# Kernel tuning notes

Measured on AMD Instinct MI355X. Metric: run time of the kernel, lower is better.

## Reference

```python
import jax, jax.numpy as jnp
import numpy as np

D = 1024
H = 16
DK = D // H


def apply_rope(x):
    # x: [B, H, T, dk]; interleaved-pair RoPE as in the torch source
    T, dim = x.shape[-2], x.shape[-1]
    inv_freq = 1.0 / (10000.0 ** (jnp.arange(0, dim, 2, dtype=x.dtype) / dim))  # [dk/2]
    pos = jnp.arange(T, dtype=x.dtype)
    sinusoid = pos[:, None] * inv_freq[None, :]  # [T, dk/2]
    sin, cos = jnp.sin(sinusoid), jnp.cos(sinusoid)
    x1, x2 = x[..., ::2], x[..., 1::2]
    rot = jnp.stack([x1 * cos - x2 * sin, x1 * sin + x2 * cos], axis=-1)
    return rot.reshape(x.shape)


def setup_inputs() -> dict:
    key = jax.random.key(0)
    k1, k2, k3, k4, k5 = jax.random.split(key, 5)
    B, T = 2, 2048
    s = 1.0 / np.sqrt(D)
    return {
        "x": jax.random.normal(k1, (B, T, D), dtype=jnp.float32),
        "W_qkv": jax.random.normal(k2, (D, 3 * D), dtype=jnp.float32) * s,
        "b_qkv": jnp.zeros((3 * D,), dtype=jnp.float32),
        "W_out": jax.random.normal(k3, (D, D), dtype=jnp.float32) * s,
        "b_out": jnp.zeros((D,), dtype=jnp.float32),
    }


def reference(x, W_qkv, b_qkv, W_out, b_out):
    B, T, C = x.shape
    qkv = x @ W_qkv + b_qkv  # [B, T, 3D]
    qkv = qkv.reshape(B, T, 3, H, DK).transpose(2, 0, 3, 1, 4)  # [3, B, H, T, dk]
    q, k, v = qkv[0], qkv[1], qkv[2]
    q, k = apply_rope(q), apply_rope(k)
    scores = jnp.einsum("bhtd,bhsd->bhts", q, k) / jnp.sqrt(jnp.asarray(DK, x.dtype))
    causal = jnp.tril(jnp.ones((T, T), dtype=bool))
    scores = jnp.where(causal, scores, jnp.asarray(-1e9, x.dtype))
    probs = jax.nn.softmax(scores, axis=-1)
    attn = jnp.einsum("bhts,bhsd->bhtd", probs, v)  # [B, H, T, dk]
    out = attn.transpose(0, 2, 1, 3).reshape(B, T, C)  # b h t d -> b t (h d)
    return out @ W_out + b_out
```

## Files before the change

### kernel.cpp

```cpp
#include <hip/hip_runtime.h>
#include <math.h>

#define DMODEL 1024
#define NHEAD  16
#define HDK    64
#define BATCH  2
#define SEQ    2048
#define MROWS  (BATCH*SEQ)
#define NQKV   (3*DMODEL)
#define LOG2_10000 13.287712379549449f
#define INV2PI 0.15915494309189535f
#define SCALE_LOG2E 0.1803368801111137f
#define M_FIX 8.0f

typedef __attribute__((ext_vector_type(8))) short bf16x8;
typedef __attribute__((ext_vector_type(4))) float f32x4;

__device__ __forceinline__ short f2bf(float f) {
    union { float f; unsigned u; } v; v.f = f;
    unsigned r = v.u + 0x7fffu + ((v.u >> 16) & 1u);
    return (short)(r >> 16);
}

__device__ __forceinline__ float fast_exp2(float x) {
#if __has_builtin(__builtin_amdgcn_exp2f)
    return __builtin_amdgcn_exp2f(x);
#else
    return exp2f(x);
#endif
}

__device__ __forceinline__ void gld_lds16(const short* g, short* l) {
    __builtin_amdgcn_global_load_lds(
        (const __attribute__((address_space(1))) void*)g,
        (__attribute__((address_space(3))) void*)l, 16, 0, 0);
}

__global__ __launch_bounds__(256) void prep_kernel(
    const float* __restrict__ x, const float* __restrict__ wqkv,
    const float* __restrict__ wout,
    short* __restrict__ xb, short* __restrict__ wqkv_t, short* __restrict__ wout_t)
{
    __shared__ short tile[32][33];
    const int tid = threadIdx.x;
    if (blockIdx.x < 2048) {
        const int i = (blockIdx.x * 256 + tid) * 8;
        float4 a = *(const float4*)(x + i);
        float4 b = *(const float4*)(x + i + 4);
        bf16x8 o;
        o[0] = f2bf(a.x); o[1] = f2bf(a.y); o[2] = f2bf(a.z); o[3] = f2bf(a.w);
        o[4] = f2bf(b.x); o[5] = f2bf(b.y); o[6] = f2bf(b.z); o[7] = f2bf(b.w);
        *(bf16x8*)(xb + i) = o;
        return;
    }
    const int bx = blockIdx.x - 2048;
    int nx = bx & 127;
    const int ky = bx >> 7;
    const float* in; short* out; int N;
    if (nx < 96) { in = wqkv; out = wqkv_t; N = NQKV; }
    else         { in = wout; out = wout_t; N = DMODEL; nx -= 96; }
    const int tx = tid & 31, ty = tid >> 5;
    const int n0 = nx * 32, k0 = ky * 32;
    #pragma unroll
    for (int i = 0; i < 32; i += 8)
        tile[ty + i][tx] = f2bf(in[(size_t)(k0 + ty + i) * N + n0 + tx]);
    __syncthreads();
    #pragma unroll
    for (int i = 0; i < 32; i += 8)
        out[(size_t)(n0 + ty + i) * DMODEL + k0 + tx] = tile[tx][ty + i];
}

__global__ __launch_bounds__(256) void qkv_gemm_kernel(
    const short* __restrict__ xb, const short* __restrict__ Wt,
    const float* __restrict__ bias,
    short* __restrict__ qd, short* __restrict__ kd, short* __restrict__ vtb)
{
    __shared__ __align__(16) short As[2][128 * 32];
    __shared__ __align__(16) short Bs[2][128 * 32];
    const int tid = threadIdx.x;
    const int lane = tid & 63, wave = tid >> 6;
    const int wm = wave & 1, wn = wave >> 1;
    const int l15 = lane & 15, quad = lane >> 4;
    const int n0 = blockIdx.x * 128, m0 = blockIdx.y * 128;
    const int srow = lane >> 2, sc = lane & 3;

    const short* gA1 = xb + (size_t)(m0 + wave * 32 + srow) * DMODEL + sc * 8;
    const short* gA2 = gA1 + (size_t)16 * DMODEL;
    const short* gB1 = Wt + (size_t)(n0 + wave * 32 + srow) * DMODEL + sc * 8;
    const short* gB2 = gB1 + (size_t)16 * DMODEL;
    const int lofsA1 = (wave * 32) * 32;
    const int lofsA2 = (wave * 32 + 16) * 32;

    f32x4 zero = {0.f, 0.f, 0.f, 0.f};
    f32x4 acc[4][4];
    #pragma unroll
    for (int i = 0; i < 4; ++i)
        #pragma unroll
        for (int j = 0; j < 4; ++j) acc[i][j] = zero;

    gld_lds16(gA1, As[0] + lofsA1);
    gld_lds16(gA2, As[0] + lofsA2);
    gld_lds16(gB1, Bs[0] + lofsA1);
    gld_lds16(gB2, Bs[0] + lofsA2);
    __syncthreads();

    for (int k = 0; k < DMODEL / 32; ++k) {
        const int cur = k & 1;
        if (k + 1 < DMODEL / 32) {
            const int kn = (k + 1) * 32;
            gld_lds16(gA1 + kn, As[cur ^ 1] + lofsA1);
            gld_lds16(gA2 + kn, As[cur ^ 1] + lofsA2);
            gld_lds16(gB1 + kn, Bs[cur ^ 1] + lofsA1);
            gld_lds16(gB2 + kn, Bs[cur ^ 1] + lofsA2);
        }
        bf16x8 af[4], bfr[4];
        #pragma unroll
        for (int i = 0; i < 4; ++i)
            af[i] = *(const bf16x8*)&As[cur][(wm * 64 + i * 16 + l15) * 32 + quad * 8];
        #pragma unroll
        for (int j = 0; j < 4; ++j)
            bfr[j] = *(const bf16x8*)&Bs[cur][(wn * 64 + j * 16 + l15) * 32 + quad * 8];
        #pragma unroll
        for (int i = 0; i < 4; ++i)
            #pragma unroll
            for (int j = 0; j < 4; ++j)
                acc[i][j] = __builtin_amdgcn_mfma_f32_16x16x32_bf16(af[i], bfr[j], acc[i][j], 0, 0, 0);
        __syncthreads();
    }

    const int which = n0 >> 10;
    float biasv[4], invf[4];
    int hh[4], dd[4];
    #pragma unroll
    for (int j = 0; j < 4; ++j) {
        const int n = n0 + wn * 64 + j * 16 + l15;
        biasv[j] = bias[n];
        hh[j] = (n & 1023) >> 6;
        dd[j] = n & 63;
        invf[j] = INV2PI * exp2f(-((float)(dd[j] & ~1) / 64.f) * LOG2_10000);
    }
    #pragma unroll
    for (int i = 0; i < 4; ++i) {
        #pragma unroll
        for (int r = 0; r < 4; ++r) {
            const int m = m0 + wm * 64 + i * 16 + quad * 4 + r;
            const int b = m >> 11, t = m & (SEQ - 1);
            #pragma unroll
            for (int j = 0; j < 4; ++j) {
                float val = acc[i][j][r] + biasv[j];
                if (which < 2) {
                    const float rev = (float)t * invf[j];
                    const float fr = rev - floorf(rev);
                    const float s = __builtin_amdgcn_sinf(fr);
                    const float c = __builtin_amdgcn_cosf(fr);
                    const float partner = __shfl_xor(val, 1);
                    val = (lane & 1) ? (partner * s + val * c) : (val * c - partner * s);
                    short* dst = (which == 0) ? qd : kd;
                    dst[((size_t)(b * NHEAD + hh[j]) * SEQ + t) * HDK + dd[j]] = f2bf(val);
                } else {
                    vtb[((size_t)(b * NHEAD + hh[j]) * HDK + dd[j]) * SEQ + t] = f2bf(val);
                }
            }
        }
    }
}

__global__ __launch_bounds__(256) void attn_mfma_kernel(
    const short* __restrict__ qd, const short* __restrict__ kd,
    const short* __restrict__ vt, short* __restrict__ od)
{
    __shared__ __align__(16) short Ks[2][2][64 * 32];
    __shared__ __align__(16) short Vs[2][2][64 * 32];
    __shared__ __align__(16) short Ps[4][16][64];
    const int tid = threadIdx.x, lane = tid & 63, w = tid >> 6;
    const int l15 = lane & 15, quad = lane >> 4;
    const int id = (int)blockIdx.x;
    const int c = id & 7, kblk = id >> 3;
    const int qt = 31 - (kblk & 31);
    const int jj = kblk >> 5;
    const int hb = c + 8 * jj;
    const int h = hb & 15, b = hb >> 4;
    const size_t base = ((size_t)(b * NHEAD + h)) * SEQ * HDK;
    const int srow = tid >> 2, sc = tid & 3;
    const int lofs = tid * 8;
    f32x4 zero = {0.f, 0.f, 0.f, 0.f};

    const short* kp0 = kd + base + (size_t)srow * HDK + sc * 8;
    const short* vp0 = vt + base + (size_t)srow * SEQ + sc * 8;
    const short* kp1 = kp0 + (size_t)64 * HDK;
    const short* vp1 = vp0 + 64;

    const int q0 = qt * 64;
    bf16x8 qf[2];
    {
        const short* qrow = qd + base + (size_t)(q0 + w * 16 + l15) * HDK;
        qf[0] = *(const bf16x8*)(qrow + quad * 8);
        qf[1] = *(const bf16x8*)(qrow + 32 + quad * 8);
    }
    float l_acc[4] = {0.f, 0.f, 0.f, 0.f};
    f32x4 o[4];
    #pragma unroll
    for (int j = 0; j < 4; ++j) o[j] = zero;

    const int nkt = qt + 1;
    const int npair = (nkt + 1) >> 1;

    bf16x8 rk[2][2], rv[2][2];
    rk[0][0] = *(const bf16x8*)kp0; rk[0][1] = *(const bf16x8*)(kp0 + 32);
    rv[0][0] = *(const bf16x8*)vp0; rv[0][1] = *(const bf16x8*)(vp0 + 32);
    rk[1][0] = *(const bf16x8*)kp1; rk[1][1] = *(const bf16x8*)(kp1 + 32);
    rv[1][0] = *(const bf16x8*)vp1; rv[1][1] = *(const bf16x8*)(vp1 + 32);

    for (int p = 0; p < npair; ++p) {
        __syncthreads();
        *(bf16x8*)&Ks[0][0][lofs] = rk[0][0]; *(bf16x8*)&Ks[0][1][lofs] = rk[0][1];
        *(bf16x8*)&Vs[0][0][lofs] = rv[0][0]; *(bf16x8*)&Vs[0][1][lofs] = rv[0][1];
        *(bf16x8*)&Ks[1][0][lofs] = rk[1][0]; *(bf16x8*)&Ks[1][1][lofs] = rk[1][1];
        *(bf16x8*)&Vs[1][0][lofs] = rv[1][0]; *(bf16x8*)&Vs[1][1][lofs] = rv[1][1];
        __syncthreads();
        if (p + 1 < npair) {
            const int sn = (2 * p + 2) * 64;
            const short* kn = kd + base + (size_t)(sn + srow) * HDK + sc * 8;
            const short* vn = vt + base + (size_t)srow * SEQ + sn + sc * 8;
            rk[0][0] = *(const bf16x8*)kn; rk[0][1] = *(const bf16x8*)(kn + 32);
            rv[0][0] = *(const bf16x8*)vn; rv[0][1] = *(const bf16x8*)(vn + 32);
            const short* kn2 = kn + (size_t)64 * HDK;
            const short* vn2 = vn + 64;
            rk[1][0] = *(const bf16x8*)kn2; rk[1][1] = *(const bf16x8*)(kn2 + 32);
            rv[1][0] = *(const bf16x8*)vn2; rv[1][1] = *(const bf16x8*)(vn2 + 32);
        }

        #pragma unroll
        for (int tt = 0; tt < 2; ++tt) {
            const int kt = 2 * p + tt;
            if (tt == 1 && kt >= nkt) break;
            f32x4 sacc[4];
            #pragma unroll
            for (int j = 0; j < 4; ++j) {
                bf16x8 kf0 = *(const bf16x8*)&Ks[tt][0][(j * 16 + l15) * 32 + quad * 8];
                bf16x8 kf1 = *(const bf16x8*)&Ks[tt][1][(j * 16 + l15) * 32 + quad * 8];
                sacc[j] = __builtin_amdgcn_mfma_f32_16x16x32_bf16(qf[0], kf0, zero, 0, 0, 0);
                sacc[j] = __builtin_amdgcn_mfma_f32_16x16x32_bf16(qf[1], kf1, sacc[j], 0, 0, 0);
            }
            if (kt == nkt - 1) {
                const int s0 = kt * 64;
                #pragma unroll
                for (int j = 0; j < 4; ++j) {
                    const int scol = s0 + j * 16 + l15;
                    #pragma unroll
                    for (int r = 0; r < 4; ++r) {
                        const int trow = q0 + w * 16 + quad * 4 + r;
                        const float sv = sacc[j][r] * SCALE_LOG2E - M_FIX;
                        const float pv = (scol > trow) ? 0.f : fast_exp2(sv);
                        l_acc[r] += pv;
                        const int pr = quad * 4 + r;
                        const int sw = (j * 2 + (l15 >> 3)) ^ (pr & 7);
                        Ps[w][pr][sw * 8 + (l15 & 7)] = f2bf(pv);
                    }
                }
            } else {
                #pragma unroll
                for (int j = 0; j < 4; ++j)
                    #pragma unroll
                    for (int r = 0; r < 4; ++r) {
                        const float pv = fast_exp2(sacc[j][r] * SCALE_LOG2E - M_FIX);
                        l_acc[r] += pv;
                        const int pr = quad * 4 + r;
                        const int sw = (j * 2 + (l15 >> 3)) ^ (pr & 7);
                        Ps[w][pr][sw * 8 + (l15 & 7)] = f2bf(pv);
                    }
            }
            bf16x8 pf0 = *(const bf16x8*)&Ps[w][l15][(quad ^ (l15 & 7)) * 8];
            bf16x8 pf1 = *(const bf16x8*)&Ps[w][l15][((4 + quad) ^ (l15 & 7)) * 8];
            #pragma unroll
            for (int j = 0; j < 4; ++j) {
                bf16x8 vf0 = *(const bf16x8*)&Vs[tt][0][(j * 16 + l15) * 32 + quad * 8];
                bf16x8 vf1 = *(const bf16x8*)&Vs[tt][1][(j * 16 + l15) * 32 + quad * 8];
                o[j] = __builtin_amdgcn_mfma_f32_16x16x32_bf16(pf0, vf0, o[j], 0, 0, 0);
                o[j] = __builtin_amdgcn_mfma_f32_16x16x32_bf16(pf1, vf1, o[j], 0, 0, 0);
            }
        }
    }

    #pragma unroll
    for (int r = 0; r < 4; ++r) {
        float sr = l_acc[r];
        #pragma unroll
        for (int off = 1; off < 16; off <<= 1) sr += __shfl_xor(sr, off);
        l_acc[r] = sr;
    }
    #pragma unroll
    for (int r = 0; r < 4; ++r) {
        const float inv = 1.f / l_acc[r];
        const int t = q0 + w * 16 + quad * 4 + r;
        #pragma unroll
        for (int j = 0; j < 4; ++j)
            od[((size_t)(b * SEQ + t) * NHEAD + h) * HDK + j * 16 + l15] =
                f2bf(o[j][r] * inv);
    }
}

__global__ __launch_bounds__(256) void out_gemm_kernel(
    const short* __restrict__ Ab, const short* __restrict__ Wt,
    const float* __restrict__ bias, float* __restrict__ out)
{
    __shared__ __align__(16) short As[2][128 * 32];
    __shared__ __align__(16) short Bs[2][64 * 32];
    const int tid = threadIdx.x;
    const int lane = tid & 63, wave = tid >> 6;
    const int wm = wave & 1, wn = wave >> 1;
    const int l15 = lane & 15, quad = lane >> 4;
    const int n0 = blockIdx.x * 64, m0 = blockIdx.y * 128;
    const int srow = lane >> 2, sc = lane & 3;

    const short* gA1 = Ab + (size_t)(m0 + wave * 32 + srow) * DMODEL + sc * 8;
    const short* gA2 = gA1 + (size_t)16 * DMODEL;
    const short* gB1 = Wt + (size_t)(n0 + wave * 16 + srow) * DMODEL + sc * 8;
    const int lofsA1 = (wave * 32) * 32;
    const int lofsA2 = (wave * 32 + 16) * 32;
    const int lofsB  = (wave * 16) * 32;

    f32x4 zero = {0.f, 0.f, 0.f, 0.f};
    f32x4 acc[4][2];
    #pragma unroll
    for (int i = 0; i < 4; ++i)
        #pragma unroll
        for (int j = 0; j < 2; ++j) acc[i][j] = zero;

    gld_lds16(gA1, As[0] + lofsA1);
    gld_lds16(gA2, As[0] + lofsA2);
    gld_lds16(gB1, Bs[0] + lofsB);
    __syncthreads();

    for (int k = 0; k < DMODEL / 32; ++k) {
        const int cur = k & 1;
        if (k + 1 < DMODEL / 32) {
            const int kn = (k + 1) * 32;
            gld_lds16(gA1 + kn, As[cur ^ 1] + lofsA1);
            gld_lds16(gA2 + kn, As[cur ^ 1] + lofsA2);
            gld_lds16(gB1 + kn, Bs[cur ^ 1] + lofsB);
        }
        bf16x8 af[4], bfr[2];
        #pragma unroll
        for (int i = 0; i < 4; ++i)
            af[i] = *(const bf16x8*)&As[cur][(wm * 64 + i * 16 + l15) * 32 + quad * 8];
        #pragma unroll
        for (int j = 0; j < 2; ++j)
            bfr[j] = *(const bf16x8*)&Bs[cur][(wn * 32 + j * 16 + l15) * 32 + quad * 8];
        #pragma unroll
        for (int i = 0; i < 4; ++i)
            #pragma unroll
            for (int j = 0; j < 2; ++j)
                acc[i][j] = __builtin_amdgcn_mfma_f32_16x16x32_bf16(af[i], bfr[j], acc[i][j], 0, 0, 0);
        __syncthreads();
    }

    #pragma unroll
    for (int j = 0; j < 2; ++j) {
        const int n = n0 + wn * 32 + j * 16 + l15;
        const float bv = bias[n];
        #pragma unroll
        for (int i = 0; i < 4; ++i)
            #pragma unroll
            for (int r = 0; r < 4; ++r) {
                const int m = m0 + wm * 64 + i * 16 + quad * 4 + r;
                out[(size_t)m * DMODEL + n] = acc[i][j][r] + bv;
            }
    }
}

extern "C" void kernel_launch(void* const* d_in, const int* in_sizes, int n_in,
                              void* d_out, int out_size, void* d_ws, size_t ws_size,
                              hipStream_t stream) {
    const float* x    = (const float*)d_in[0];
    const float* Wqkv = (const float*)d_in[1];
    const float* bqkv = (const float*)d_in[2];
    const float* Wout = (const float*)d_in[3];
    const float* bout = (const float*)d_in[4];
    float* out = (float*)d_out;

    short* ws = (short*)d_ws;
    short* xb     = ws;
    short* wqkv_t = xb + (size_t)4 * 1024 * 1024;
    short* wout_t = wqkv_t + (size_t)3 * 1024 * 1024;
    short* qd     = wout_t + (size_t)1024 * 1024;
    short* kd     = qd + (size_t)4 * 1024 * 1024;
    short* vtb    = kd + (size_t)4 * 1024 * 1024;
    short* attn   = vtb + (size_t)4 * 1024 * 1024;

    prep_kernel<<<2048 + 4096, 256, 0, stream>>>(x, Wqkv, Wout, xb, wqkv_t, wout_t);

    qkv_gemm_kernel<<<dim3(NQKV / 128, MROWS / 128), 256, 0, stream>>>(
        xb, wqkv_t, bqkv, qd, kd, vtb);

    attn_mfma_kernel<<<1024, 256, 0, stream>>>(qd, kd, vtb, attn);

    out_gemm_kernel<<<dim3(DMODEL / 64, MROWS / 128), 256, 0, stream>>>(
        attn, wout_t, bout, out);
}
```

Baseline: 203.1 us.

## Split attention KV tiles across two wave groups with LDS reduction and swizzle

Doubles the attention block to 512 threads. The two groups of four waves each process alternating 64-key tiles of the same query tile, and their partial O and row sums are combined through shared memory at the end. The K/V shared-memory layout gets an XOR swizzle on both the stores and the MFMA reads to reduce bank conflicts. This raises the wave count per query tile and parallelism along the KV axis, at the cost of an extra reduction, extra barriers, and more LDS traffic; with fixed-max softmax the partial sums add directly.

```diff
diff --git a/kernel.cpp b/kernel.cpp
--- a/kernel.cpp
+++ b/kernel.cpp
@@ -165,15 +165,17 @@
     }
 }
 
-__global__ __launch_bounds__(256) void attn_mfma_kernel(
+__global__ __launch_bounds__(512) void attn_mfma_kernel(
     const short* __restrict__ qd, const short* __restrict__ kd,
     const short* __restrict__ vt, short* __restrict__ od)
 {
     __shared__ __align__(16) short Ks[2][2][64 * 32];
     __shared__ __align__(16) short Vs[2][2][64 * 32];
-    __shared__ __align__(16) short Ps[4][16][64];
+    __shared__ __align__(16) short Ps[8][16][64];
     const int tid = threadIdx.x, lane = tid & 63, w = tid >> 6;
     const int l15 = lane & 15, quad = lane >> 4;
+    const int par = w >> 2;
+    const int ws = w & 3;
     const int id = (int)blockIdx.x;
     const int c = id & 7, kblk = id >> 3;
     const int qt = 31 - (kblk & 31);
@@ -181,19 +183,20 @@
     const int hb = c + 8 * jj;
     const int h = hb & 15, b = hb >> 4;
     const size_t base = ((size_t)(b * NHEAD + h)) * SEQ * HDK;
-    const int srow = tid >> 2, sc = tid & 3;
-    const int lofs = tid * 8;
+    const int stid = tid & 255;
+    const int hi = tid >> 8;
+    const int srow = stid >> 2, sc = stid & 3;
+    const int lofs = srow * 32 + (sc ^ ((srow >> 1) & 3)) * 8;
+    const int rdx = (l15 >> 1) & 3;
     f32x4 zero = {0.f, 0.f, 0.f, 0.f};
 
-    const short* kp0 = kd + base + (size_t)srow * HDK + sc * 8;
-    const short* vp0 = vt + base + (size_t)srow * SEQ + sc * 8;
-    const short* kp1 = kp0 + (size_t)64 * HDK;
-    const short* vp1 = vp0 + 64;
+    const short* kp = kd + base + (size_t)(hi * 64 + srow) * HDK + sc * 8;
+    const short* vp = vt + base + (size_t)srow * SEQ + hi * 64 + sc * 8;
 
     const int q0 = qt * 64;
     bf16x8 qf[2];
     {
-        const short* qrow = qd + base + (size_t)(q0 + w * 16 + l15) * HDK;
+        const short* qrow = qd + base + (size_t)(q0 + ws * 16 + l15) * HDK;
         qf[0] = *(const bf16x8*)(qrow + quad * 8);
         qf[1] = *(const bf16x8*)(qrow + 32 + quad * 8);
     }
@@ -205,40 +208,33 @@
     const int nkt = qt + 1;
     const int npair = (nkt + 1) >> 1;
 
-    bf16x8 rk[2][2], rv[2][2];
-    rk[0][0] = *(const bf16x8*)kp0; rk[0][1] = *(const bf16x8*)(kp0 + 32);
-    rv[0][0] = *(const bf16x8*)vp0; rv[0][1] = *(const bf16x8*)(vp0 + 32);
-    rk[1][0] = *(const bf16x8*)kp1; rk[1][1] = *(const bf16x8*)(kp1 + 32);
-    rv[1][0] = *(const bf16x8*)vp1; rv[1][1] = *(const bf16x8*)(vp1 + 32);
+    bf16x8 rk[2], rv[2];
+    rk[0] = *(const bf16x8*)kp; rk[1] = *(const bf16x8*)(kp + 32);
+    rv[0] = *(const bf16x8*)vp; rv[1] = *(const bf16x8*)(vp + 32);
 
     for (int p = 0; p < npair; ++p) {
         __syncthreads();
-        *(bf16x8*)&Ks[0][0][lofs] = rk[0][0]; *(bf16x8*)&Ks[0][1][lofs] = rk[0][1];
-        *(bf16x8*)&Vs[0][0][lofs] = rv[0][0]; *(bf16x8*)&Vs[0][1][lofs] = rv[0][1];
-        *(bf16x8*)&Ks[1][0][lofs] = rk[1][0]; *(bf16x8*)&Ks[1][1][lofs] = rk[1][1];
-        *(bf16x8*)&Vs[1][0][lofs] = rv[1][0]; *(bf16x8*)&Vs[1][1][lofs] = rv[1][1];
+        *(bf16x8*)&Ks[hi][0][lofs] = rk[0];
+        *(bf16x8*)&Ks[hi][1][lofs] = rk[1];
+        *(bf16x8*)&Vs[hi][0][lofs] = rv[0];
+        *(bf16x8*)&Vs[hi][1][lofs] = rv[1];
         __syncthreads();
         if (p + 1 < npair) {
             const int sn = (2 * p + 2) * 64;
-            const short* kn = kd + base + (size_t)(sn + srow) * HDK + sc * 8;
-            const short* vn = vt + base + (size_t)srow * SEQ + sn + sc * 8;
-            rk[0][0] = *(const bf16x8*)kn; rk[0][1] = *(const bf16x8*)(kn + 32);
-            rv[0][0] = *(const bf16x8*)vn; rv[0][1] = *(const bf16x8*)(vn + 32);
-            const short* kn2 = kn + (size_t)64 * HDK;
-            const short* vn2 = vn + 64;
-            rk[1][0] = *(const bf16x8*)kn2; rk[1][1] = *(const bf16x8*)(kn2 + 32);
-            rv[1][0] = *(const bf16x8*)vn2; rv[1][1] = *(const bf16x8*)(vn2 + 32);
-        }
-
-        #pragma unroll
-        for (int tt = 0; tt < 2; ++tt) {
-            const int kt = 2 * p + tt;
-            if (tt == 1 && kt >= nkt) break;
+            const short* kn = kp + (size_t)sn * HDK;
+            const short* vn = vp + sn;
+            rk[0] = *(const bf16x8*)kn; rk[1] = *(const bf16x8*)(kn + 32);
+            rv[0] = *(const bf16x8*)vn; rv[1] = *(const bf16x8*)(vn + 32);
+        }
+
+        const int kt = 2 * p + par;
+        if (kt < nkt) {
             f32x4 sacc[4];
             #pragma unroll
             for (int j = 0; j < 4; ++j) {
-                bf16x8 kf0 = *(const bf16x8*)&Ks[tt][0][(j * 16 + l15) * 32 + quad * 8];
-                bf16x8 kf1 = *(const bf16x8*)&Ks[tt][1][(j * 16 + l15) * 32 + quad * 8];
+                const int ro = (j * 16 + l15) * 32 + ((quad ^ rdx)) * 8;
+                bf16x8 kf0 = *(const bf16x8*)&Ks[par][0][ro];
+                bf16x8 kf1 = *(const bf16x8*)&Ks[par][1][ro];
                 sacc[j] = __builtin_amdgcn_mfma_f32_16x16x32_bf16(qf[0], kf0, zero, 0, 0, 0);
                 sacc[j] = __builtin_amdgcn_mfma_f32_16x16x32_bf16(qf[1], kf1, sacc[j], 0, 0, 0);
             }
@@ -249,7 +245,7 @@
                     const int scol = s0 + j * 16 + l15;
                     #pragma unroll
                     for (int r = 0; r < 4; ++r) {
-                        const int trow = q0 + w * 16 + quad * 4 + r;
+                        const int trow = q0 + ws * 16 + quad * 4 + r;
                         const float sv = sacc[j][r] * SCALE_LOG2E - M_FIX;
                         const float pv = (scol > trow) ? 0.f : fast_exp2(sv);
                         l_acc[r] += pv;
@@ -274,29 +270,55 @@
             bf16x8 pf1 = *(const bf16x8*)&Ps[w][l15][((4 + quad) ^ (l15 & 7)) * 8];
             #pragma unroll
             for (int j = 0; j < 4; ++j) {
-                bf16x8 vf0 = *(const bf16x8*)&Vs[tt][0][(j * 16 + l15) * 32 + quad * 8];
-                bf16x8 vf1 = *(const bf16x8*)&Vs[tt][1][(j * 16 + l15) * 32 + quad * 8];
+                const int ro = (j * 16 + l15) * 32 + ((quad ^ rdx)) * 8;
+                bf16x8 vf0 = *(const bf16x8*)&Vs[par][0][ro];
+                bf16x8 vf1 = *(const bf16x8*)&Vs[par][1][ro];
                 o[j] = __builtin_amdgcn_mfma_f32_16x16x32_bf16(pf0, vf0, o[j], 0, 0, 0);
                 o[j] = __builtin_amdgcn_mfma_f32_16x16x32_bf16(pf1, vf1, o[j], 0, 0, 0);
             }
         }
     }
 
-    #pragma unroll
-    for (int r = 0; r < 4; ++r) {
-        float sr = l_acc[r];
-        #pragma unroll
-        for (int off = 1; off < 16; off <<= 1) sr += __shfl_xor(sr, off);
-        l_acc[r] = sr;
-    }
-    #pragma unroll
-    for (int r = 0; r < 4; ++r) {
-        const float inv = 1.f / l_acc[r];
-        const int t = q0 + w * 16 + quad * 4 + r;
+    __syncthreads();
+    float* ob = (float*)&Ks[0][0][0];
+    float* lb = (float*)&Vs[0][0][0];
+    if (par == 1) {
+        const int bi = (ws * 64 + lane) * 16;
         #pragma unroll
         for (int j = 0; j < 4; ++j)
-            od[((size_t)(b * SEQ + t) * NHEAD + h) * HDK + j * 16 + l15] =
-                f2bf(o[j][r] * inv);
+            #pragma unroll
+            for (int r = 0; r < 4; ++r) ob[bi + j * 4 + r] = o[j][r];
+        const int li = (ws * 64 + lane) * 4;
+        #pragma unroll
+        for (int r = 0; r < 4; ++r) lb[li + r] = l_acc[r];
+    }
+    __syncthreads();
+    if (par == 0) {
+        const int bi = (ws * 64 + lane) * 16;
+        #pragma unroll
+        for (int j = 0; j < 4; ++j)
+            #pragma unroll
+            for (int r = 0; r < 4; ++r) o[j][r] += ob[bi + j * 4 + r];
+        const int li = (ws * 64 + lane) * 4;
+        #pragma unroll
+        for (int r = 0; r < 4; ++r) l_acc[r] += lb[li + r];
+
+        #pragma unroll
+        for (int r = 0; r < 4; ++r) {
+            float sr = l_acc[r];
+            #pragma unroll
+            for (int off = 1; off < 16; off <<= 1) sr += __shfl_xor(sr, off);
+            l_acc[r] = sr;
+        }
+        #pragma unroll
+        for (int r = 0; r < 4; ++r) {
+            const float inv = 1.f / l_acc[r];
+            const int t = q0 + ws * 16 + quad * 4 + r;
+            #pragma unroll
+            for (int j = 0; j < 4; ++j)
+                od[((size_t)(b * SEQ + t) * NHEAD + h) * HDK + j * 16 + l15] =
+                    f2bf(o[j][r] * inv);
+        }
     }
 }
 
@@ -393,7 +415,7 @@
     qkv_gemm_kernel<<<dim3(NQKV / 128, MROWS / 128), 256, 0, stream>>>(
         xb, wqkv_t, bqkv, qd, kd, vtb);
 
-    attn_mfma_kernel<<<1024, 256, 0, stream>>>(qd, kd, vtb, attn);
+    attn_mfma_kernel<<<1024, 512, 0, stream>>>(qd, kd, vtb, attn);
 
     out_gemm_kernel<<<dim3(DMODEL / 64, MROWS / 128), 256, 0, stream>>>(
         attn, wout_t, bout, out);
```

New measurement: 196.9 us. 3.1% less time.
